# Performance work log

Hardware: AMD Instinct MI355X
Metric: run time of the kernel (lower is better)

The kernel has to match this reference:

```python
import jax, jax.numpy as jnp
import numpy as np

B, S, D, H = 16, 512, 768, 12
DH = D // H


def setup_inputs() -> dict:
    key = jax.random.key(0)
    ks = jax.random.split(key, 12)
    hidden_states = jax.random.normal(ks[0], (B, S, D), dtype=jnp.float32)
    # additive padding mask: 0 for valid, -10000 for padded tail tokens
    lengths = jax.random.randint(ks[1], (B,), S // 2, S + 1)
    pad = (jnp.arange(S)[None, :] >= lengths[:, None]).astype(jnp.float32)
    attention_mask = (pad * -10000.0)[:, None, None, :]  # [B,1,1,S]
    # row-stochastic graph prior over codes
    pr = jax.random.uniform(ks[2], (B, S, S), dtype=jnp.float32)
    prior = pr / jnp.sum(pr, axis=-1, keepdims=True)
    s = 0.02
    params = dict(
        Wq=jax.random.normal(ks[3], (D, D)) * s, bq=jnp.zeros((D,)),
        Wk=jax.random.normal(ks[4], (D, D)) * s, bk=jnp.zeros((D,)),
        Wv=jax.random.normal(ks[5], (D, D)) * s, bv=jnp.zeros((D,)),
        Wg=jax.random.normal(ks[6], (D, 2)) * s, bg=jnp.zeros((2,)),
        Wo=jax.random.normal(ks[7], (D, D)) * s, bo=jnp.zeros((D,)),
        gamma=jnp.ones((D,)), beta=jnp.zeros((D,)),
    )
    return dict(hidden_states=hidden_states, attention_mask=attention_mask,
                prior=prior, **params)


def _layer_norm(x, gamma, beta, eps=1e-5):
    mu = jnp.mean(x, axis=-1, keepdims=True)
    var = jnp.mean(jnp.square(x - mu), axis=-1, keepdims=True)
    return (x - mu) * jax.lax.rsqrt(var + eps) * gamma + beta


def reference(hidden_states, attention_mask, prior,
              Wq, bq, Wk, bk, Wv, bv, Wg, bg, Wo, bo, gamma, beta):
    b, s, d = hidden_states.shape
    # project and split heads: [B,S,H,DH]
    q = (hidden_states @ Wq + bq).reshape(b, s, H, DH)
    k = (hidden_states @ Wk + bk).reshape(b, s, H, DH)
    v = (hidden_states @ Wv + bv).reshape(b, s, H, DH)
    scores = jnp.einsum('bshd,bthd->bhst', q, k) / jnp.sqrt(jnp.float32(DH))
    scores = scores + attention_mask  # broadcast [B,1,1,S]
    probs = jax.nn.softmax(scores, axis=-1)  # [B,H,S,S]
    # gate: avg-pool over valid tokens, softmax(linear/2)
    valid = (attention_mask.squeeze((1, 2)) == 0.0).astype(hidden_states.dtype)  # [B,S]
    denom = jnp.maximum(jnp.sum(valid, axis=1, keepdims=True), 1.0)
    h_pool = jnp.sum(hidden_states * valid[:, :, None], axis=1) / denom  # [B,D]
    gate = jax.nn.softmax((h_pool @ Wg + bg) / 2.0, axis=-1)  # [B,2]
    probs = probs * gate[:, 0, None, None, None] + prior[:, None, :, :] * gate[:, 1, None, None, None]
    ctx = jnp.einsum('bhst,bthd->bshd', probs, v).reshape(b, s, d)
    out = jax.nn.relu(ctx @ Wo + bo)
    out = _layer_norm(out + hidden_states, gamma, beta)
    return out
```

## Files before the change

### kernel.cpp

```cpp
#include <hip/hip_runtime.h>

#define NB_ 16
#define S_ 512
#define D_ 768
#define H_ 12
#define DH_ 64
#define QT_ 64
#define KT_ 128
#define LDQ_ 1536

typedef __attribute__((ext_vector_type(8))) short bf16x8;
typedef __attribute__((ext_vector_type(4))) float f32x4;
typedef unsigned short ushort_t;

__device__ __forceinline__ unsigned short f2bf(float f){
  unsigned int u = __float_as_uint(f);
  u += 0x7fffu + ((u >> 16) & 1u);
  return (unsigned short)(u >> 16);
}
__device__ __forceinline__ float bf2f(unsigned short s){
  return __uint_as_float(((unsigned int)s) << 16);
}
__device__ __forceinline__ unsigned int pack2(float a, float b){
  return (unsigned int)f2bf(a) | ((unsigned int)f2bf(b) << 16);
}
__device__ __forceinline__ void gld16(const ushort_t* g, ushort_t* l){
  __builtin_amdgcn_global_load_lds((const __attribute__((address_space(1))) unsigned int*)g,
                                   (__attribute__((address_space(3))) unsigned int*)l, 16, 0, 0);
}

__global__ __launch_bounds__(256) void k_setup(
    const float* __restrict__ hs, const float* __restrict__ mask,
    const float* __restrict__ W0, const float* __restrict__ W1,
    const float* __restrict__ W2, const float* __restrict__ W3,
    const float* __restrict__ b0, const float* __restrict__ b1, const float* __restrict__ b2,
    ushort_t* __restrict__ hsb, ushort_t* __restrict__ wt, float* __restrict__ bqkv,
    float* __restrict__ partial, float* __restrict__ pcnt)
{
  __shared__ float t[32][33];
  const int bx = blockIdx.x, tid = threadIdx.x;
  if (bx < 512){
    int chunk = bx & 31, b = bx >> 5;
    const float* mrow = mask + b * S_ + chunk * 16;
    const float* base = hs + ((size_t)b * S_ + chunk * 16) * D_;
    ushort_t* obase = hsb + ((size_t)b * S_ + chunk * 16) * D_;
    float a0 = 0.f, a1 = 0.f, a2 = 0.f, cnt = 0.f;
#pragma unroll 2
    for (int s = 0; s < 16; s++){
      const float* r = base + (size_t)s * D_;
      float x0 = r[tid], x1 = r[tid + 256], x2 = r[tid + 512];
      ushort_t* o = obase + (size_t)s * D_;
      o[tid] = f2bf(x0); o[tid + 256] = f2bf(x1); o[tid + 512] = f2bf(x2);
      if (mrow[s] == 0.0f){ a0 += x0; a1 += x1; a2 += x2; cnt += 1.0f; }
    }
    float* o = partial + (size_t)(b * 32 + chunk) * D_;
    o[tid] = a0; o[tid + 256] = a1; o[tid + 512] = a2;
    if (tid == 0) pcnt[b * 32 + chunk] = cnt;
  } else if (bx < 512 + 2304){
    int idx = bx - 512;
    int z = idx / 576, rem = idx - z * 576;
    int ky = rem / 24, nx = rem - ky * 24;
    const float* W = (z == 0) ? W0 : (z == 1) ? W1 : (z == 2) ? W2 : W3;
    ushort_t* o = wt + (size_t)z * D_ * D_;
    int j = tid & 31, i0 = tid >> 5;
    int kb = ky * 32, nb = nx * 32;
#pragma unroll
    for (int r = 0; r < 4; r++){
      int i = i0 + r * 8;
      t[i][j] = W[(size_t)(kb + i) * D_ + nb + j];
    }
    __syncthreads();
#pragma unroll
    for (int r = 0; r < 4; r++){
      int i = i0 + r * 8;
      o[(size_t)(nb + i) * D_ + kb + j] = f2bf(t[j][i]);
    }
  } else {
    int i = (bx - 2816) * 256 + tid;
    if (i < 3 * D_){
      float v = (i < D_) ? b0[i] : (i < 2 * D_) ? b1[i - D_] : b2[i - 2 * D_];
      bqkv[i] = v;
    }
  }
}

__global__ __launch_bounds__(256) void k_pool2(const float* __restrict__ partial, const float* __restrict__ pcnt,
                                               const float* __restrict__ Wg, const float* __restrict__ bg,
                                               float* __restrict__ gate){
  int b = blockIdx.x, tid = threadIdx.x;
  __shared__ float red[256];
  __shared__ float hp[768];
  float a0 = 0.f, a1 = 0.f, a2 = 0.f;
#pragma unroll
  for (int c = 0; c < 32; c++){
    const float* p = partial + (size_t)(b * 32 + c) * D_;
    a0 += p[tid]; a1 += p[tid + 256]; a2 += p[tid + 512];
  }
  float denom = 0.f;
#pragma unroll
  for (int c = 0; c < 32; c++) denom += pcnt[b * 32 + c];
  float inv = 1.0f / fmaxf(denom, 1.0f);
  hp[tid] = a0 * inv; hp[tid + 256] = a1 * inv; hp[tid + 512] = a2 * inv;
  __syncthreads();
  float p0 = 0.f, p1 = 0.f;
  for (int d = tid; d < D_; d += 256){ p0 += hp[d] * Wg[d * 2]; p1 += hp[d] * Wg[d * 2 + 1]; }
  red[tid] = p0; __syncthreads();
  for (int o = 128; o > 0; o >>= 1){ if (tid < o) red[tid] += red[tid + o]; __syncthreads(); }
  float z0 = red[0]; __syncthreads();
  red[tid] = p1; __syncthreads();
  for (int o = 128; o > 0; o >>= 1){ if (tid < o) red[tid] += red[tid + o]; __syncthreads(); }
  float z1 = red[0];
  if (tid == 0){
    z0 = (z0 + bg[0]) * 0.5f; z1 = (z1 + bg[1]) * 0.5f;
    float m = fmaxf(z0, z1);
    float e0 = __expf(z0 - m), e1 = __expf(z1 - m);
    float ssum = e0 + e1;
    gate[b * 2] = e0 / ssum; gate[b * 2 + 1] = e1 / ssum;
  }
}

template<int OUTBF16, int RELU, int RESID, int AFP32, int MAP, int VSPLIT>
__global__ __launch_bounds__(256) void k_gemm_bt(
    const void* __restrict__ Ap, long sA, int lda,
    const ushort_t* __restrict__ Bm, long sB, int ldb,
    void* __restrict__ Cp, long sC, int ldc, void* __restrict__ Cp2,
    const float* __restrict__ bias,
    const float* __restrict__ resid, float alpha, int K)
{
  __shared__ ushort_t As[128 * 64];
  __shared__ ushort_t Bs[128 * 64];
  int z, bm, bn;
  if (MAP == 2){ z = blockIdx.x; bm = blockIdx.y; bn = blockIdx.z; }
  else if (MAP == 1){ z = blockIdx.z; bm = blockIdx.x; bn = blockIdx.y; }
  else { z = blockIdx.z; bm = blockIdx.y; bn = blockIdx.x; }
  const ushort_t* Ab = AFP32 ? nullptr : ((const ushort_t*)Ap + (size_t)z * sA);
  const float*    Af = AFP32 ? ((const float*)Ap + (size_t)z * sA) : nullptr;
  const ushort_t* Bb = Bm + (size_t)z * sB;
  const long coff = (long)z * sC;
  const int tid = threadIdx.x;
  const int m0 = bm * 128, n0 = bn * 128;
  const int wid = tid >> 6, lane = tid & 63;
  const int quad = lane >> 4, l16 = lane & 15;
  const int wm = wid >> 1, wn = wid & 1;
  const int sw = l16 & 7;

  f32x4 acc[4][4];
#pragma unroll
  for (int i = 0; i < 4; i++)
#pragma unroll
    for (int j = 0; j < 4; j++) acc[i][j] = (f32x4){0.f, 0.f, 0.f, 0.f};

  for (int k0 = 0; k0 < K; k0 += 64){
#pragma unroll
    for (int c = 0; c < 4; c++){
      int idx = tid + c * 256;
      int row = idx >> 3, p = idx & 7;
      int cg = p ^ (row & 7);
      if (AFP32){
        const float* src = Af + (size_t)(m0 + row) * lda + k0 + cg * 8;
        float4 f0 = *(const float4*)src;
        float4 f1 = *(const float4*)(src + 4);
        uint4 pk;
        pk.x = pack2(f0.x, f0.y);
        pk.y = pack2(f0.z, f0.w);
        pk.z = pack2(f1.x, f1.y);
        pk.w = pack2(f1.z, f1.w);
        *(uint4*)(&As[idx * 8]) = pk;
      } else {
        gld16(Ab + (size_t)(m0 + row) * lda + k0 + cg * 8, &As[idx * 8]);
      }
    }
#pragma unroll
    for (int c = 0; c < 4; c++){
      int idx = tid + c * 256;
      int row = idx >> 3, p = idx & 7;
      int cg = p ^ (row & 7);
      gld16(Bb + (size_t)(n0 + row) * ldb + k0 + cg * 8, &Bs[idx * 8]);
    }
    __syncthreads();
#pragma unroll
    for (int ks = 0; ks < 2; ks++){
      bf16x8 af[4], bfv[4];
#pragma unroll
      for (int mi = 0; mi < 4; mi++){
        int row = wm * 64 + mi * 16 + l16;
        af[mi] = *(const bf16x8*)(&As[(row * 8 + ((ks * 4 + quad) ^ sw)) * 8]);
      }
#pragma unroll
      for (int ni = 0; ni < 4; ni++){
        int row = wn * 64 + ni * 16 + l16;
        bfv[ni] = *(const bf16x8*)(&Bs[(row * 8 + ((ks * 4 + quad) ^ sw)) * 8]);
      }
#pragma unroll
      for (int mi = 0; mi < 4; mi++)
#pragma unroll
        for (int ni = 0; ni < 4; ni++)
          acc[mi][ni] = __builtin_amdgcn_mfma_f32_16x16x32_bf16(af[mi], bfv[ni], acc[mi][ni], 0, 0, 0);
    }
    __syncthreads();
  }

  if (VSPLIT && n0 >= 1536){
    ushort_t* vtp = (ushort_t*)Cp2;
    const int bb = m0 >> 9;
#pragma unroll
    for (int mi = 0; mi < 4; mi++){
#pragma unroll
      for (int ni = 0; ni < 4; ni++){
        int col = n0 + wn * 64 + ni * 16 + l16;
        float bcol = bias[col];
        int hh = (col - 1536) >> 6, dh = (col - 1536) & 63;
        int trow = (m0 & 511) + wm * 64 + mi * 16 + quad * 4;
        uint2 pk;
        pk.x = pack2(acc[mi][ni][0] + bcol, acc[mi][ni][1] + bcol);
        pk.y = pack2(acc[mi][ni][2] + bcol, acc[mi][ni][3] + bcol);
        *(uint2*)(vtp + ((size_t)(bb * H_ + hh) * DH_ + dh) * S_ + trow) = pk;
      }
    }
    return;
  }

#pragma unroll
  for (int mi = 0; mi < 4; mi++){
#pragma unroll
    for (int ni = 0; ni < 4; ni++){
      int col = n0 + wn * 64 + ni * 16 + l16;
      float bcol = bias ? bias[col] : 0.0f;
#pragma unroll
      for (int r = 0; r < 4; r++){
        int row = m0 + wm * 64 + mi * 16 + quad * 4 + r;
        float v = acc[mi][ni][r] * alpha + bcol;
        if (RELU) v = fmaxf(v, 0.0f);
        if (RESID) v += resid[(size_t)row * ldc + col];
        long idx = coff + (long)row * ldc + col;
        if (OUTBF16) ((ushort_t*)Cp)[idx] = f2bf(v);
        else         ((float*)Cp)[idx] = v;
      }
    }
  }
}

__global__ __launch_bounds__(256) void k_flash(
    const ushort_t* __restrict__ qkv,
    const ushort_t* __restrict__ vt,
    const ushort_t* __restrict__ priorctx,
    const float* __restrict__ mask,
    const float* __restrict__ gate,
    ushort_t* __restrict__ ctx)
{
  __shared__ ushort_t Ks[KT_ * 64];
  __shared__ ushort_t Vs[DH_ * 128];
  __shared__ ushort_t Ps[QT_ * 136];
  __shared__ float rs[QT_];
  const int z = blockIdx.x, b = z / H_, h = z - b * H_;
  const int q0 = blockIdx.y * QT_;
  const int tid = threadIdx.x;
  const int wid = tid >> 6, lane = tid & 63, quad = lane >> 4, l16 = lane & 15;

  bf16x8 bq[4][2];
#pragma unroll
  for (int ni = 0; ni < 4; ni++)
#pragma unroll
    for (int ks = 0; ks < 2; ks++)
      bq[ni][ks] = *(const bf16x8*)(qkv + ((size_t)(b * S_ + q0 + ni * 16 + l16)) * LDQ_
                                    + h * DH_ + ks * 32 + quad * 8);
  if (tid < QT_) rs[tid] = 0.f;

  f32x4 accv[4];
#pragma unroll
  for (int ni = 0; ni < 4; ni++) accv[ni] = (f32x4){0.f, 0.f, 0.f, 0.f};

  for (int t0 = 0; t0 < S_; t0 += KT_){
    if (mask[b * S_ + t0] != 0.0f) break;
#pragma unroll
    for (int c = 0; c < 4; c++){
      int idx = tid + c * 256;
      int row = idx >> 3, p = idx & 7;
      int cg = p ^ (row & 7);
      gld16(qkv + ((size_t)(b * S_ + t0 + row)) * LDQ_ + D_ + h * DH_ + cg * 8, &Ks[idx * 8]);
    }
#pragma unroll
    for (int c = 0; c < 4; c++){
      int idx = tid + c * 256;
      int row = idx >> 4, p = idx & 15;
      int cg = p ^ (row & 15);
      gld16(vt + (size_t)z * (DH_ * S_) + (size_t)row * S_ + t0 + cg * 8, &Vs[idx * 8]);
    }
    __syncthreads();

    f32x4 accs[2][4];
#pragma unroll
    for (int mi = 0; mi < 2; mi++)
#pragma unroll
      for (int ni = 0; ni < 4; ni++) accs[mi][ni] = (f32x4){0.f, 0.f, 0.f, 0.f};
#pragma unroll
    for (int ks = 0; ks < 2; ks++){
      bf16x8 ak[2];
#pragma unroll
      for (int mi = 0; mi < 2; mi++){
        int row = wid * 32 + mi * 16 + l16;
        ak[mi] = *(const bf16x8*)(&Ks[(row * 8 + ((ks * 4 + quad) ^ (l16 & 7))) * 8]);
      }
#pragma unroll
      for (int mi = 0; mi < 2; mi++)
#pragma unroll
        for (int ni = 0; ni < 4; ni++)
          accs[mi][ni] = __builtin_amdgcn_mfma_f32_16x16x32_bf16(ak[mi], bq[ni][ks], accs[mi][ni], 0, 0, 0);
    }

    float mv[2][4];
#pragma unroll
    for (int mi = 0; mi < 2; mi++)
#pragma unroll
      for (int r = 0; r < 4; r++)
        mv[mi][r] = mask[b * S_ + t0 + wid * 32 + mi * 16 + quad * 4 + r];
    float rowpart[4] = {0.f, 0.f, 0.f, 0.f};
#pragma unroll
    for (int mi = 0; mi < 2; mi++){
#pragma unroll
      for (int ni = 0; ni < 4; ni++){
        float e0 = __expf(accs[mi][ni][0] * 0.125f + mv[mi][0]);
        float e1 = __expf(accs[mi][ni][1] * 0.125f + mv[mi][1]);
        float e2 = __expf(accs[mi][ni][2] * 0.125f + mv[mi][2]);
        float e3 = __expf(accs[mi][ni][3] * 0.125f + mv[mi][3]);
        rowpart[ni] += (e0 + e1) + (e2 + e3);
        uint2 pk;
        pk.x = pack2(e0, e1);
        pk.y = pack2(e2, e3);
        *(uint2*)(&Ps[(ni * 16 + l16) * 136 + wid * 32 + mi * 16 + quad * 4]) = pk;
      }
    }
#pragma unroll
    for (int ni = 0; ni < 4; ni++){
      rowpart[ni] += __shfl_xor(rowpart[ni], 16);
      rowpart[ni] += __shfl_xor(rowpart[ni], 32);
    }
    if (lane < 16){
#pragma unroll
      for (int ni = 0; ni < 4; ni++) atomicAdd(&rs[ni * 16 + l16], rowpart[ni]);
    }
    __syncthreads();

#pragma unroll
    for (int ks = 0; ks < 4; ks++){
      bf16x8 ap = *(const bf16x8*)(&Ps[(wid * 16 + l16) * 136 + ks * 32 + quad * 8]);
#pragma unroll
      for (int ni = 0; ni < 4; ni++){
        bf16x8 bv8 = *(const bf16x8*)(&Vs[((ni * 16 + l16) * 16 + ((ks * 4 + quad) ^ l16)) * 8]);
        accv[ni] = __builtin_amdgcn_mfma_f32_16x16x32_bf16(ap, bv8, accv[ni], 0, 0, 0);
      }
    }
    __syncthreads();
  }

  const float g0 = gate[b * 2], g1 = gate[b * 2 + 1];
#pragma unroll
  for (int ni = 0; ni < 4; ni++){
#pragma unroll
    for (int r = 0; r < 4; r++){
      int q = wid * 16 + quad * 4 + r;
      int dh = ni * 16 + l16;
      float scl = g0 / rs[q];
      size_t idx = ((size_t)(b * S_ + q0 + q)) * D_ + h * DH_ + dh;
      float v = accv[ni][r] * scl + g1 * bf2f(priorctx[idx]);
      ctx[idx] = f2bf(v);
    }
  }
}

__global__ __launch_bounds__(256) void k_ln(float* __restrict__ out, const float* __restrict__ gamma,
                                            const float* __restrict__ beta){
  __shared__ float red[256];
  int row = blockIdx.x, tid = threadIdx.x;
  float* p = out + (size_t)row * D_;
  float x0 = p[tid], x1 = p[tid + 256], x2 = p[tid + 512];
  red[tid] = x0 + x1 + x2; __syncthreads();
  for (int o = 128; o > 0; o >>= 1){ if (tid < o) red[tid] += red[tid + o]; __syncthreads(); }
  float mu = red[0] * (1.0f / 768.0f);
  __syncthreads();
  float d0 = x0 - mu, d1 = x1 - mu, d2 = x2 - mu;
  red[tid] = d0 * d0 + d1 * d1 + d2 * d2; __syncthreads();
  for (int o = 128; o > 0; o >>= 1){ if (tid < o) red[tid] += red[tid + o]; __syncthreads(); }
  float rsv = rsqrtf(red[0] * (1.0f / 768.0f) + 1e-5f);
  p[tid]       = d0 * rsv * gamma[tid]       + beta[tid];
  p[tid + 256] = d1 * rsv * gamma[tid + 256] + beta[tid + 256];
  p[tid + 512] = d2 * rsv * gamma[tid + 512] + beta[tid + 512];
}

extern "C" void kernel_launch(void* const* d_in, const int* in_sizes, int n_in,
                              void* d_out, int out_size, void* d_ws, size_t ws_size,
                              hipStream_t stream){
  const float* hs    = (const float*)d_in[0];
  const float* mask  = (const float*)d_in[1];
  const float* prior = (const float*)d_in[2];
  const float* Wq = (const float*)d_in[3];  const float* bq = (const float*)d_in[4];
  const float* Wk = (const float*)d_in[5];  const float* bk = (const float*)d_in[6];
  const float* Wv = (const float*)d_in[7];  const float* bv = (const float*)d_in[8];
  const float* Wg = (const float*)d_in[9];  const float* bg = (const float*)d_in[10];
  const float* Wo = (const float*)d_in[11]; const float* bo = (const float*)d_in[12];
  const float* gamma = (const float*)d_in[13]; const float* beta = (const float*)d_in[14];
  float* out = (float*)d_out;

  size_t off = 0;
  auto alloc = [&](size_t bytes) -> char* {
    char* p = (char*)d_ws + off;
    off += (bytes + 255) & ~(size_t)255;
    return p;
  };
  const size_t HSD = (size_t)NB_ * S_ * D_;
  ushort_t* hsb     = (ushort_t*)alloc(HSD * 2);
  ushort_t* qkvb    = (ushort_t*)alloc(HSD * 2 * 2);
  ushort_t* vtb     = (ushort_t*)alloc(HSD * 2);
  ushort_t* wt      = (ushort_t*)alloc((size_t)4 * D_ * D_ * 2);
  ushort_t* priorctx= (ushort_t*)alloc(HSD * 2);
  ushort_t* ctx     = (ushort_t*)alloc(HSD * 2);
  float*    bqkv    = (float*)alloc((size_t)3 * D_ * 4);
  float*    gate    = (float*)alloc(256);
  float*    partial = (float*)alloc((size_t)NB_ * 32 * D_ * 4);
  float*    pcnt    = (float*)alloc((size_t)NB_ * 32 * 4);

  k_setup<<<dim3(2825), 256, 0, stream>>>(hs, mask, Wq, Wk, Wv, Wo, bq, bk, bv,
                                          hsb, wt, bqkv, partial, pcnt);
  k_pool2<<<dim3(NB_), 256, 0, stream>>>(partial, pcnt, Wg, bg, gate);
  k_gemm_bt<1, 0, 0, 0, 1, 1><<<dim3(64, 18, 1), 256, 0, stream>>>(
      hsb, 0, D_, wt, 0, D_, qkvb, 0, LDQ_, vtb, bqkv, nullptr, 1.0f, D_);
  k_gemm_bt<1, 0, 0, 1, 2, 0><<<dim3(16, 4, 6), 256, 0, stream>>>(
      prior, (long)S_ * S_, S_, vtb, (long)H_ * DH_ * S_, S_,
      priorctx, (long)S_ * D_, D_, nullptr, nullptr, nullptr, 1.0f, S_);
  k_flash<<<dim3(NB_ * H_, S_ / QT_), 256, 0, stream>>>(
      qkvb, vtb, priorctx, mask, gate, ctx);
  k_gemm_bt<0, 1, 1, 0, 1, 0><<<dim3(64, 6, 1), 256, 0, stream>>>(
      ctx, 0, D_, wt + 3 * (size_t)D_ * D_, 0, D_, out, 0, D_, nullptr, bo, hs, 1.0f, D_);
  k_ln<<<dim3(NB_ * S_), 256, 0, stream>>>(out, gamma, beta);
}
```

Before: 275.0 us.

## Double-buffer GEMM LDS tiles and pre-convert prior to bf16 in setup

The GEMM kernel now double-buffers its A and B tiles in LDS, issuing async global-to-LDS loads for the next k-slice while MFMAs run on the current one. Wait counts are explicit, and MFMA sections get raised wave priority. The fp32 prior conversion moves out of the GEMM into extra setup blocks that write a bf16 copy into the ctx buffer, so every GEMM uses the direct-to-LDS load path. This doubles LDS use per block and adds a separate pass over prior that writes a full bf16 copy.

```diff
diff --git a/kernel.cpp b/kernel.cpp
--- a/kernel.cpp
+++ b/kernel.cpp
@@ -30,12 +30,12 @@
 }
 
 __global__ __launch_bounds__(256) void k_setup(
-    const float* __restrict__ hs, const float* __restrict__ mask,
+    const float* __restrict__ hs, const float* __restrict__ mask, const float* __restrict__ prior,
     const float* __restrict__ W0, const float* __restrict__ W1,
     const float* __restrict__ W2, const float* __restrict__ W3,
     const float* __restrict__ b0, const float* __restrict__ b1, const float* __restrict__ b2,
     ushort_t* __restrict__ hsb, ushort_t* __restrict__ wt, float* __restrict__ bqkv,
-    float* __restrict__ partial, float* __restrict__ pcnt)
+    float* __restrict__ partial, float* __restrict__ pcnt, ushort_t* __restrict__ priorb)
 {
   __shared__ float t[32][33];
   const int bx = blockIdx.x, tid = threadIdx.x;
@@ -75,12 +75,23 @@
       int i = i0 + r * 8;
       o[(size_t)(nb + i) * D_ + kb + j] = f2bf(t[j][i]);
     }
-  } else {
+  } else if (bx < 2825){
     int i = (bx - 2816) * 256 + tid;
     if (i < 3 * D_){
       float v = (i < D_) ? b0[i] : (i < 2 * D_) ? b1[i - D_] : b2[i - 2 * D_];
       bqkv[i] = v;
     }
+  } else {
+    size_t i = (size_t)(bx - 2825) * 4096 + (size_t)tid * 16;
+    const float4* s4 = (const float4*)(prior + i);
+    float4 f0 = s4[0], f1 = s4[1], f2 = s4[2], f3 = s4[3];
+    uint4 p0, p1;
+    p0.x = pack2(f0.x, f0.y); p0.y = pack2(f0.z, f0.w);
+    p0.z = pack2(f1.x, f1.y); p0.w = pack2(f1.z, f1.w);
+    p1.x = pack2(f2.x, f2.y); p1.y = pack2(f2.z, f2.w);
+    p1.z = pack2(f3.x, f3.y); p1.w = pack2(f3.z, f3.w);
+    *(uint4*)(priorb + i) = p0;
+    *(uint4*)(priorb + i + 8) = p1;
   }
 }
 
@@ -119,22 +130,21 @@
   }
 }
 
-template<int OUTBF16, int RELU, int RESID, int AFP32, int MAP, int VSPLIT>
-__global__ __launch_bounds__(256) void k_gemm_bt(
-    const void* __restrict__ Ap, long sA, int lda,
+template<int OUTBF16, int RELU, int RESID, int MAP, int VSPLIT>
+__global__ __launch_bounds__(256, 2) void k_gemm_bt(
+    const ushort_t* __restrict__ Am, long sA, int lda,
     const ushort_t* __restrict__ Bm, long sB, int ldb,
     void* __restrict__ Cp, long sC, int ldc, void* __restrict__ Cp2,
     const float* __restrict__ bias,
     const float* __restrict__ resid, float alpha, int K)
 {
-  __shared__ ushort_t As[128 * 64];
-  __shared__ ushort_t Bs[128 * 64];
+  __shared__ ushort_t As[2][128 * 64];
+  __shared__ ushort_t Bs[2][128 * 64];
   int z, bm, bn;
   if (MAP == 2){ z = blockIdx.x; bm = blockIdx.y; bn = blockIdx.z; }
   else if (MAP == 1){ z = blockIdx.z; bm = blockIdx.x; bn = blockIdx.y; }
   else { z = blockIdx.z; bm = blockIdx.y; bn = blockIdx.x; }
-  const ushort_t* Ab = AFP32 ? nullptr : ((const ushort_t*)Ap + (size_t)z * sA);
-  const float*    Af = AFP32 ? ((const float*)Ap + (size_t)z * sA) : nullptr;
+  const ushort_t* Ab = Am + (size_t)z * sA;
   const ushort_t* Bb = Bm + (size_t)z * sB;
   const long coff = (long)z * sC;
   const int tid = threadIdx.x;
@@ -144,60 +154,66 @@
   const int wm = wid >> 1, wn = wid & 1;
   const int sw = l16 & 7;
 
-  f32x4 acc[4][4];
-#pragma unroll
-  for (int i = 0; i < 4; i++)
-#pragma unroll
-    for (int j = 0; j < 4; j++) acc[i][j] = (f32x4){0.f, 0.f, 0.f, 0.f};
-
-  for (int k0 = 0; k0 < K; k0 += 64){
+  auto stage = [&](int buf, int k0){
 #pragma unroll
     for (int c = 0; c < 4; c++){
       int idx = tid + c * 256;
       int row = idx >> 3, p = idx & 7;
       int cg = p ^ (row & 7);
-      if (AFP32){
-        const float* src = Af + (size_t)(m0 + row) * lda + k0 + cg * 8;
-        float4 f0 = *(const float4*)src;
-        float4 f1 = *(const float4*)(src + 4);
-        uint4 pk;
-        pk.x = pack2(f0.x, f0.y);
-        pk.y = pack2(f0.z, f0.w);
-        pk.z = pack2(f1.x, f1.y);
-        pk.w = pack2(f1.z, f1.w);
-        *(uint4*)(&As[idx * 8]) = pk;
-      } else {
-        gld16(Ab + (size_t)(m0 + row) * lda + k0 + cg * 8, &As[idx * 8]);
-      }
+      gld16(Ab + (size_t)(m0 + row) * lda + k0 + cg * 8, &As[buf][idx * 8]);
     }
 #pragma unroll
     for (int c = 0; c < 4; c++){
       int idx = tid + c * 256;
       int row = idx >> 3, p = idx & 7;
       int cg = p ^ (row & 7);
-      gld16(Bb + (size_t)(n0 + row) * ldb + k0 + cg * 8, &Bs[idx * 8]);
-    }
-    __syncthreads();
+      gld16(Bb + (size_t)(n0 + row) * ldb + k0 + cg * 8, &Bs[buf][idx * 8]);
+    }
+  };
+
+  f32x4 acc[4][4];
+#pragma unroll
+  for (int i = 0; i < 4; i++)
+#pragma unroll
+    for (int j = 0; j < 4; j++) acc[i][j] = (f32x4){0.f, 0.f, 0.f, 0.f};
+
+  stage(0, 0);
+  int cur = 0;
+  for (int k0 = 0; k0 < K; k0 += 64){
+    if (k0 + 64 < K){
+      stage(cur ^ 1, k0 + 64);
+      __builtin_amdgcn_sched_barrier(0);
+      asm volatile("s_waitcnt vmcnt(8)" ::: "memory");
+    } else {
+      __builtin_amdgcn_sched_barrier(0);
+      asm volatile("s_waitcnt vmcnt(0)" ::: "memory");
+    }
+    __builtin_amdgcn_sched_barrier(0);
+    __builtin_amdgcn_s_barrier();
 #pragma unroll
     for (int ks = 0; ks < 2; ks++){
       bf16x8 af[4], bfv[4];
 #pragma unroll
       for (int mi = 0; mi < 4; mi++){
         int row = wm * 64 + mi * 16 + l16;
-        af[mi] = *(const bf16x8*)(&As[(row * 8 + ((ks * 4 + quad) ^ sw)) * 8]);
+        af[mi] = *(const bf16x8*)(&As[cur][(row * 8 + ((ks * 4 + quad) ^ sw)) * 8]);
       }
 #pragma unroll
       for (int ni = 0; ni < 4; ni++){
         int row = wn * 64 + ni * 16 + l16;
-        bfv[ni] = *(const bf16x8*)(&Bs[(row * 8 + ((ks * 4 + quad) ^ sw)) * 8]);
-      }
+        bfv[ni] = *(const bf16x8*)(&Bs[cur][(row * 8 + ((ks * 4 + quad) ^ sw)) * 8]);
+      }
+      __builtin_amdgcn_s_setprio(1);
 #pragma unroll
       for (int mi = 0; mi < 4; mi++)
 #pragma unroll
         for (int ni = 0; ni < 4; ni++)
           acc[mi][ni] = __builtin_amdgcn_mfma_f32_16x16x32_bf16(af[mi], bfv[ni], acc[mi][ni], 0, 0, 0);
-    }
-    __syncthreads();
+      __builtin_amdgcn_s_setprio(0);
+    }
+    __builtin_amdgcn_sched_barrier(0);
+    __builtin_amdgcn_s_barrier();
+    cur ^= 1;
   }
 
   if (VSPLIT && n0 >= 1536){
@@ -418,18 +434,19 @@
   float*    gate    = (float*)alloc(256);
   float*    partial = (float*)alloc((size_t)NB_ * 32 * D_ * 4);
   float*    pcnt    = (float*)alloc((size_t)NB_ * 32 * 4);
-
-  k_setup<<<dim3(2825), 256, 0, stream>>>(hs, mask, Wq, Wk, Wv, Wo, bq, bk, bv,
-                                          hsb, wt, bqkv, partial, pcnt);
+  ushort_t* priorb  = ctx;
+
+  k_setup<<<dim3(3849), 256, 0, stream>>>(hs, mask, prior, Wq, Wk, Wv, Wo, bq, bk, bv,
+                                          hsb, wt, bqkv, partial, pcnt, priorb);
   k_pool2<<<dim3(NB_), 256, 0, stream>>>(partial, pcnt, Wg, bg, gate);
-  k_gemm_bt<1, 0, 0, 0, 1, 1><<<dim3(64, 18, 1), 256, 0, stream>>>(
+  k_gemm_bt<1, 0, 0, 1, 1><<<dim3(64, 18, 1), 256, 0, stream>>>(
       hsb, 0, D_, wt, 0, D_, qkvb, 0, LDQ_, vtb, bqkv, nullptr, 1.0f, D_);
-  k_gemm_bt<1, 0, 0, 1, 2, 0><<<dim3(16, 4, 6), 256, 0, stream>>>(
-      prior, (long)S_ * S_, S_, vtb, (long)H_ * DH_ * S_, S_,
+  k_gemm_bt<1, 0, 0, 2, 0><<<dim3(16, 4, 6), 256, 0, stream>>>(
+      priorb, (long)S_ * S_, S_, vtb, (long)H_ * DH_ * S_, S_,
       priorctx, (long)S_ * D_, D_, nullptr, nullptr, nullptr, 1.0f, S_);
   k_flash<<<dim3(NB_ * H_, S_ / QT_), 256, 0, stream>>>(
       qkvb, vtb, priorctx, mask, gate, ctx);
-  k_gemm_bt<0, 1, 1, 0, 1, 0><<<dim3(64, 6, 1), 256, 0, stream>>>(
+  k_gemm_bt<0, 1, 1, 1, 0><<<dim3(64, 6, 1), 256, 0, stream>>>(
       ctx, 0, D_, wt + 3 * (size_t)D_ * D_, 0, D_, out, 0, D_, nullptr, bo, hs, 1.0f, D_);
   k_ln<<<dim3(NB_ * S_), 256, 0, stream>>>(out, gamma, beta);
 }
```

After: 265.4 us. -3.5%, faster.
